# Kernel optimization log

Hardware: AMD Instinct MI355X
Metric: run time of the kernel (lower is better)

Reference implementation:

```python
import jax, jax.numpy as jnp
import numpy as np

N, D, H = 24, 256, 8
F = D // H  # 32


def setup_inputs() -> dict:
    key = jax.random.key(0)
    ks = jax.random.split(key, 9)
    T = 8192
    x = jax.random.normal(ks[0], (T, N * D), dtype=jnp.float32)
    s = 0.02
    # Joint-specific query weights: (H, N, D, F); shared K/V: (H, D, F)
    Wq = jax.random.normal(ks[1], (H, N, D, F), dtype=jnp.float32) * s
    bq = jax.random.normal(ks[2], (H, N, F), dtype=jnp.float32) * s
    Wk = jax.random.normal(ks[3], (H, D, F), dtype=jnp.float32) * s
    bk = jax.random.normal(ks[4], (H, F), dtype=jnp.float32) * s
    Wv = jax.random.normal(ks[5], (H, D, F), dtype=jnp.float32) * s
    bv = jax.random.normal(ks[6], (H, F), dtype=jnp.float32) * s
    gamma = jnp.ones((N * D,), dtype=jnp.float32)
    beta = jnp.zeros((N * D,), dtype=jnp.float32)
    return {"x": x, "Wq": Wq, "bq": bq, "Wk": Wk, "bk": bk,
            "Wv": Wv, "bv": bv, "gamma": gamma, "beta": beta}


def reference(x, Wq, bq, Wk, bk, Wv, bv, gamma, beta):
    T = x.shape[0]
    xr = x.reshape(T, N, D)                                   # (T, N, D)
    # Shared K/V per head, joint-specific Q per head
    k = jnp.einsum('tnd,hdf->thnf', xr, Wk) + bk[None, :, None, :]
    v = jnp.einsum('tnd,hdf->thnf', xr, Wv) + bv[None, :, None, :]
    q = jnp.einsum('tnd,hndf->thnf', xr, Wq) + bq[None, :, :, :]
    scores = jnp.einsum('thnf,thmf->thnm', q, k) / jnp.sqrt(jnp.float32(F))
    attn = jax.nn.softmax(scores, axis=-1)                    # (T, H, N, N)
    out = jnp.einsum('thnm,thmf->thnf', attn, v)              # (T, H, N, F)
    # Concat heads -> (T, N, H*F) = (T, N, D)
    out = jnp.transpose(out, (0, 2, 1, 3)).reshape(T, N * D)
    # Dropout is identity in eval mode; residual + LayerNorm over N*D
    y = x + out
    mu = jnp.mean(y, axis=-1, keepdims=True)
    var = jnp.mean((y - mu) ** 2, axis=-1, keepdims=True)
    y = (y - mu) * jax.lax.rsqrt(var + 1e-5)
    return y * gamma + beta
```

## Files before the change

### kernel.cpp

```cpp
#include <hip/hip_runtime.h>

#define NT 8192
#define NJ 24
#define DD 256
#define NH 8
#define FF 32
#define C3 768

typedef __attribute__((ext_vector_type(8))) _Float16 f16x8;
typedef __attribute__((ext_vector_type(2))) _Float16 half2v;
typedef __attribute__((ext_vector_type(4))) float f32x4;

__device__ __forceinline__ unsigned short f2h(float f) {
    union { _Float16 h; unsigned short u; } c;
    c.h = (_Float16)f;
    return c.u;
}

__device__ __forceinline__ float dot2(unsigned int a, unsigned int b, float c) {
#if __has_builtin(__builtin_amdgcn_fdot2)
    return __builtin_amdgcn_fdot2(__builtin_bit_cast(half2v, a),
                                  __builtin_bit_cast(half2v, b), c, false);
#else
    half2v ha = __builtin_bit_cast(half2v, a);
    half2v hb = __builtin_bit_cast(half2v, b);
    return c + (float)ha[0] * (float)hb[0] + (float)ha[1] * (float)hb[1];
#endif
}

__device__ __forceinline__ void gload16(const void* g, void* l) {
    __builtin_amdgcn_global_load_lds(
        (const __attribute__((address_space(1))) unsigned int*)g,
        (__attribute__((address_space(3))) unsigned int*)l, 16, 0, 0);
}

__global__ void pack_w(const float* __restrict__ Wq, const float* __restrict__ Wk,
                       const float* __restrict__ Wv, unsigned short* __restrict__ wbt) {
    size_t idx = (size_t)blockIdx.x * 256 + threadIdx.x;
    const size_t total = (size_t)NJ * C3 * DD;
    if (idx >= total) return;
    int d = idx & 255;
    int rest = (int)(idx >> 8);
    int c = rest % C3;
    int n = rest / C3;
    float v;
    if (c < 256) {
        int h = c >> 5, f = c & 31;
        v = Wq[((((size_t)h * NJ + n) * DD) + d) * FF + f];
    } else if (c < 512) {
        int cc = c - 256; int h = cc >> 5, f = cc & 31;
        v = Wk[(((size_t)h * DD) + d) * FF + f];
    } else {
        int cc = c - 512; int h = cc >> 5, f = cc & 31;
        v = Wv[(((size_t)h * DD) + d) * FF + f];
    }
    wbt[idx] = f2h(v);
}

__global__ void pack_b(const float* __restrict__ bq, const float* __restrict__ bk,
                       const float* __restrict__ bv, float* __restrict__ bias) {
    int idx = blockIdx.x * 256 + threadIdx.x;
    if (idx >= NJ * C3) return;
    int c = idx % C3;
    int n = idx / C3;
    float v;
    if (c < 256) {
        int h = c >> 5, f = c & 31;
        v = bq[((h * NJ + n) * FF) + f];
    } else if (c < 512) {
        int cc = c - 256; int h = cc >> 5, f = cc & 31;
        v = bk[h * FF + f];
    } else {
        int cc = c - 512; int h = cc >> 5, f = cc & 31;
        v = bv[h * FF + f];
    }
    bias[idx] = v;
}

__global__ void pack_x(const float* __restrict__ x, unsigned short* __restrict__ xb) {
    size_t idx = (size_t)blockIdx.x * 256 + threadIdx.x;
    const size_t total = (size_t)NT * NJ * DD / 4;
    if (idx >= total) return;
    float4 v = ((const float4*)x)[idx];
    ushort4 h;
    h.x = f2h(v.x); h.y = f2h(v.y); h.z = f2h(v.z); h.w = f2h(v.w);
    ((ushort4*)xb)[idx] = h;
}

#define BM 128
#define BN 128

__global__ __launch_bounds__(256, 3)
void gemm_qkv(const unsigned short* __restrict__ xb, const unsigned short* __restrict__ wbt,
              const float* __restrict__ bias, unsigned short* __restrict__ qkv,
              int t0, int mbs) {
    const int nwg = gridDim.x;
    const int cpx = nwg >> 3;
    const int bid = blockIdx.x;
    const int swz = (bid & 7) * cpx + (bid >> 3);
    const int nb = swz % 6;
    const int rest = swz / 6;
    const int mb = rest % mbs;
    const int nj = rest / mbs;

    const int tid = threadIdx.x;
    const int wave = tid >> 6, lane = tid & 63;

    __shared__ unsigned short As[BM * 64];
    __shared__ unsigned short Bs[BN * 64];

    f32x4 acc[4][4];
    #pragma unroll
    for (int i = 0; i < 4; ++i)
        #pragma unroll
        for (int j = 0; j < 4; ++j)
            #pragma unroll
            for (int r = 0; r < 4; ++r) acc[i][j][r] = 0.f;

    const int trow0 = t0 + mb * BM;
    const char* srcA = (const char*)(xb + (size_t)trow0 * (NJ * DD) + nj * DD);
    const char* srcB = (const char*)(wbt + ((size_t)nj * C3 + (size_t)nb * BN) * DD);

    const int rg = lane >> 3;
    const int sc = (lane & 7) ^ rg;

    const int wr = (wave >> 1) * 64;
    const int wc = (wave & 1) * 64;
    const int lr = lane & 15;
    const int g  = lane >> 4;

    for (int kb = 0; kb < 4; ++kb) {
        #pragma unroll
        for (int i = 0; i < 4; ++i) {
            int row0 = wave * 32 + i * 8;
            gload16(srcA + (size_t)(row0 + rg) * (NJ * DD * 2) + kb * 128 + sc * 16,
                    (char*)As + row0 * 128);
        }
        #pragma unroll
        for (int i = 0; i < 4; ++i) {
            int row0 = wave * 32 + i * 8;
            gload16(srcB + (size_t)(row0 + rg) * (DD * 2) + kb * 128 + sc * 16,
                    (char*)Bs + row0 * 128);
        }
        __syncthreads();

        #pragma unroll
        for (int kk = 0; kk < 2; ++kk) {
            f16x8 a[4], b[4];
            #pragma unroll
            for (int i = 0; i < 4; ++i) {
                int row = wr + i * 16 + lr;
                int c16 = (kk * 4 + g) ^ (row & 7);
                a[i] = *(const f16x8*)((const char*)As + row * 128 + c16 * 16);
            }
            #pragma unroll
            for (int j = 0; j < 4; ++j) {
                int row = wc + j * 16 + lr;
                int c16 = (kk * 4 + g) ^ (row & 7);
                b[j] = *(const f16x8*)((const char*)Bs + row * 128 + c16 * 16);
            }
            #pragma unroll
            for (int i = 0; i < 4; ++i)
                #pragma unroll
                for (int j = 0; j < 4; ++j)
                    acc[i][j] = __builtin_amdgcn_mfma_f32_16x16x32_f16(a[i], b[j], acc[i][j], 0, 0, 0);
        }
        __syncthreads();
    }

    const int ln = lane & 15;
    const int lq = (lane >> 4) * 4;
    float bv[4];
    #pragma unroll
    for (int j = 0; j < 4; ++j)
        bv[j] = bias[nj * C3 + nb * BN + wc + j * 16 + ln];
    #pragma unroll
    for (int i = 0; i < 4; ++i) {
        #pragma unroll
        for (int r = 0; r < 4; ++r) {
            int trow = mb * BM + wr + i * 16 + lq + r;
            size_t base = ((size_t)trow * NJ + nj) * C3 + (size_t)nb * BN;
            #pragma unroll
            for (int j = 0; j < 4; ++j) {
                float val = acc[i][j][r] + bv[j];
                qkv[base + wc + j * 16 + ln] = f2h(val);
            }
        }
    }
}

__global__ __launch_bounds__(256, 4)
void attn_ln(const unsigned short* __restrict__ qkv, const float* __restrict__ x,
             const float* __restrict__ gamma, const float* __restrict__ beta,
             float* __restrict__ out, int t0) {
    const int tloc = blockIdx.x;
    const int t = t0 + tloc;
    const int tid = threadIdx.x;
    const int wave = tid >> 6, lane = tid & 63;

    __shared__ __align__(16) unsigned short kv[NJ * 512];
    __shared__ float red[8];
    __shared__ float stats[2];
    float4* os4 = (float4*)kv;

    const uint4* tok = (const uint4*)(qkv + (size_t)tloc * (NJ * C3));

    #pragma unroll
    for (int j = 0; j < 6; ++j) {
        int idx = tid + j * 256;
        int m = idx >> 6, r = idx & 63;
        ((uint4*)kv)[(m << 6) + r] = tok[m * 96 + 32 + r];
    }

    const bool active = tid < NH * NJ;
    const int h = active ? (tid / NJ) : 0;
    const int n = active ? (tid - h * NJ) : 0;
    unsigned int qp[16];
    if (active) {
        const uint4* qsrc = tok + n * 96 + h * 4;
        #pragma unroll
        for (int jj = 0; jj < 4; ++jj) {
            uint4 w = qsrc[jj];
            qp[jj * 4 + 0] = w.x; qp[jj * 4 + 1] = w.y;
            qp[jj * 4 + 2] = w.z; qp[jj * 4 + 3] = w.w;
        }
    }
    __syncthreads();

    half2v o2[16];
    if (active) {
        const unsigned short* kbase = kv + h * FF;
        float s[NJ];
        float mx = -1e30f;
        #pragma unroll
        for (int m = 0; m < NJ; ++m) {
            const uint4* kp = (const uint4*)(kbase + m * 512);
            float a = 0.f;
            #pragma unroll
            for (int jj = 0; jj < 4; ++jj) {
                uint4 kw = kp[jj];
                a = dot2(kw.x, qp[jj * 4 + 0], a);
                a = dot2(kw.y, qp[jj * 4 + 1], a);
                a = dot2(kw.z, qp[jj * 4 + 2], a);
                a = dot2(kw.w, qp[jj * 4 + 3], a);
            }
            a *= 0.17677669529663687f;
            s[m] = a;
            mx = fmaxf(mx, a);
        }
        float sum = 0.f;
        #pragma unroll
        for (int m = 0; m < NJ; ++m) { s[m] = __expf(s[m] - mx); sum += s[m]; }
        float inv = 1.f / sum;
        #pragma unroll
        for (int k = 0; k < 16; ++k) o2[k] = half2v{(_Float16)0.f, (_Float16)0.f};
        const unsigned short* vbase = kv + 256 + h * FF;
        #pragma unroll
        for (int m = 0; m < NJ; ++m) {
            float wm = s[m] * inv;
            half2v wv = __builtin_bit_cast(half2v, __builtin_amdgcn_cvt_pkrtz(wm, wm));
            const uint4* vp = (const uint4*)(vbase + m * 512);
            #pragma unroll
            for (int jj = 0; jj < 4; ++jj) {
                uint4 vw = vp[jj];
                o2[jj * 4 + 0] += __builtin_bit_cast(half2v, vw.x) * wv;
                o2[jj * 4 + 1] += __builtin_bit_cast(half2v, vw.y) * wv;
                o2[jj * 4 + 2] += __builtin_bit_cast(half2v, vw.z) * wv;
                o2[jj * 4 + 3] += __builtin_bit_cast(half2v, vw.w) * wv;
            }
        }
    }
    __syncthreads();
    if (active) {
        int base4 = n * 64 + h * 8;
        #pragma unroll
        for (int jj = 0; jj < 8; ++jj) {
            int wi = base4 + jj;
            int sw = wi ^ ((wi >> 6) & 7);
            os4[sw] = make_float4((float)o2[jj * 2][0], (float)o2[jj * 2][1],
                                  (float)o2[jj * 2 + 1][0], (float)o2[jj * 2 + 1][1]);
        }
    }
    __syncthreads();

    const float4* x4 = (const float4*)(x + (size_t)t * (NJ * DD));
    float4 yv[6];
    float sum = 0.f, sq = 0.f;
    #pragma unroll
    for (int j = 0; j < 6; ++j) {
        int ri = tid + j * 256;
        float4 a = x4[ri];
        float4 b = os4[ri ^ ((ri >> 6) & 7)];
        float4 y;
        y.x = a.x + b.x; y.y = a.y + b.y; y.z = a.z + b.z; y.w = a.w + b.w;
        yv[j] = y;
        sum += y.x + y.y + y.z + y.w;
        sq  += y.x * y.x + y.y * y.y + y.z * y.z + y.w * y.w;
    }
    #pragma unroll
    for (int off = 32; off > 0; off >>= 1) {
        sum += __shfl_down(sum, off);
        sq  += __shfl_down(sq, off);
    }
    if (lane == 0) { red[wave] = sum; red[4 + wave] = sq; }
    __syncthreads();
    if (tid == 0) {
        float s = red[0] + red[1] + red[2] + red[3];
        float q = red[4] + red[5] + red[6] + red[7];
        float mu = s * (1.f / 6144.f);
        float var = q * (1.f / 6144.f) - mu * mu;
        stats[0] = mu;
        stats[1] = rsqrtf(var + 1e-5f);
    }
    __syncthreads();
    const float mu = stats[0], rs = stats[1];
    const float4* g4 = (const float4*)gamma;
    const float4* b4 = (const float4*)beta;
    float4* out4 = (float4*)(out + (size_t)t * (NJ * DD));
    #pragma unroll
    for (int j = 0; j < 6; ++j) {
        float4 g = g4[tid + j * 256];
        float4 bb = b4[tid + j * 256];
        float4 y = yv[j];
        y.x = (y.x - mu) * rs * g.x + bb.x;
        y.y = (y.y - mu) * rs * g.y + bb.y;
        y.z = (y.z - mu) * rs * g.z + bb.z;
        y.w = (y.w - mu) * rs * g.w + bb.w;
        out4[tid + j * 256] = y;
    }
}

extern "C" void kernel_launch(void* const* d_in, const int* in_sizes, int n_in,
                              void* d_out, int out_size, void* d_ws, size_t ws_size,
                              hipStream_t stream) {
    const float* x     = (const float*)d_in[0];
    const float* Wq    = (const float*)d_in[1];
    const float* bq    = (const float*)d_in[2];
    const float* Wk    = (const float*)d_in[3];
    const float* bk    = (const float*)d_in[4];
    const float* Wv    = (const float*)d_in[5];
    const float* bv    = (const float*)d_in[6];
    const float* gamma = (const float*)d_in[7];
    const float* beta  = (const float*)d_in[8];
    float* out = (float*)d_out;

    char* ws = (char*)d_ws;
    const size_t wbt_bytes  = (size_t)NJ * C3 * DD * 2;
    const size_t bias_bytes = (size_t)NJ * C3 * 4;
    const size_t xb_bytes   = (size_t)NT * NJ * DD * 2;
    unsigned short* wbt = (unsigned short*)ws;
    float* bias = (float*)(ws + wbt_bytes);
    unsigned short* xb  = (unsigned short*)(ws + wbt_bytes + bias_bytes);
    unsigned short* qkv = (unsigned short*)(ws + wbt_bytes + bias_bytes + xb_bytes);

    const size_t fixed = wbt_bytes + bias_bytes + xb_bytes;
    size_t avail = (ws_size > fixed) ? ws_size - fixed : 0;
    int chunk = NT;
    while (chunk > BM && (size_t)chunk * NJ * C3 * 2 > avail) chunk >>= 1;

    const size_t wtotal = (size_t)NJ * C3 * DD;
    pack_w<<<dim3((unsigned)((wtotal + 255) / 256)), dim3(256), 0, stream>>>(Wq, Wk, Wv, wbt);
    pack_b<<<dim3((NJ * C3 + 255) / 256), dim3(256), 0, stream>>>(bq, bk, bv, bias);
    const size_t xtotal4 = (size_t)NT * NJ * DD / 4;
    pack_x<<<dim3((unsigned)((xtotal4 + 255) / 256)), dim3(256), 0, stream>>>(x, xb);

    for (int t0 = 0; t0 < NT; t0 += chunk) {
        int mbs = chunk / BM;
        gemm_qkv<<<dim3(6 * mbs * NJ), dim3(256), 0, stream>>>(xb, wbt, bias, qkv, t0, mbs);
        attn_ln<<<dim3(chunk), dim3(256), 0, stream>>>(qkv, x, gamma, beta, out, t0);
    }
}
```

Baseline: 620.1 us.

## Fuse fp32-to-fp16 conversion of x into GEMM A-tile load and merge pack kernels

Removes the separate pack_x pass that wrote a half-precision copy of x. The QKV GEMM now loads fp32 x directly with float4 reads, converts to fp16 in registers and stores into swizzled LDS. Bias packing is folded into the weight pack kernel, saving a launch. This drops a full read and write of x through HBM. In exchange, each A tile is read at fp32 width six times (once per N-block) through synchronous register loads instead of async global_load_lds, which may stall the GEMM.

```diff
diff --git a/kernel.cpp b/kernel.cpp
--- a/kernel.cpp
+++ b/kernel.cpp
@@ -34,8 +34,10 @@
         (__attribute__((address_space(3))) unsigned int*)l, 16, 0, 0);
 }
 
-__global__ void pack_w(const float* __restrict__ Wq, const float* __restrict__ Wk,
-                       const float* __restrict__ Wv, unsigned short* __restrict__ wbt) {
+__global__ void pack_wb(const float* __restrict__ Wq, const float* __restrict__ Wk,
+                        const float* __restrict__ Wv, unsigned short* __restrict__ wbt,
+                        const float* __restrict__ bq, const float* __restrict__ bk,
+                        const float* __restrict__ bv, float* __restrict__ bias) {
     size_t idx = (size_t)blockIdx.x * 256 + threadIdx.x;
     const size_t total = (size_t)NJ * C3 * DD;
     if (idx >= total) return;
@@ -55,43 +57,30 @@
         v = Wv[(((size_t)h * DD) + d) * FF + f];
     }
     wbt[idx] = f2h(v);
-}
-
-__global__ void pack_b(const float* __restrict__ bq, const float* __restrict__ bk,
-                       const float* __restrict__ bv, float* __restrict__ bias) {
-    int idx = blockIdx.x * 256 + threadIdx.x;
-    if (idx >= NJ * C3) return;
-    int c = idx % C3;
-    int n = idx / C3;
-    float v;
-    if (c < 256) {
-        int h = c >> 5, f = c & 31;
-        v = bq[((h * NJ + n) * FF) + f];
-    } else if (c < 512) {
-        int cc = c - 256; int h = cc >> 5, f = cc & 31;
-        v = bk[h * FF + f];
-    } else {
-        int cc = c - 512; int h = cc >> 5, f = cc & 31;
-        v = bv[h * FF + f];
-    }
-    bias[idx] = v;
-}
-
-__global__ void pack_x(const float* __restrict__ x, unsigned short* __restrict__ xb) {
-    size_t idx = (size_t)blockIdx.x * 256 + threadIdx.x;
-    const size_t total = (size_t)NT * NJ * DD / 4;
-    if (idx >= total) return;
-    float4 v = ((const float4*)x)[idx];
-    ushort4 h;
-    h.x = f2h(v.x); h.y = f2h(v.y); h.z = f2h(v.z); h.w = f2h(v.w);
-    ((ushort4*)xb)[idx] = h;
+
+    if (idx < NJ * C3) {
+        int cb = (int)(idx % C3);
+        int nb2 = (int)(idx / C3);
+        float bvv;
+        if (cb < 256) {
+            int h = cb >> 5, f = cb & 31;
+            bvv = bq[((h * NJ + nb2) * FF) + f];
+        } else if (cb < 512) {
+            int cc = cb - 256; int h = cc >> 5, f = cc & 31;
+            bvv = bk[h * FF + f];
+        } else {
+            int cc = cb - 512; int h = cc >> 5, f = cc & 31;
+            bvv = bv[h * FF + f];
+        }
+        bias[idx] = bvv;
+    }
 }
 
 #define BM 128
 #define BN 128
 
 __global__ __launch_bounds__(256, 3)
-void gemm_qkv(const unsigned short* __restrict__ xb, const unsigned short* __restrict__ wbt,
+void gemm_qkv(const float* __restrict__ x, const unsigned short* __restrict__ wbt,
               const float* __restrict__ bias, unsigned short* __restrict__ qkv,
               int t0, int mbs) {
     const int nwg = gridDim.x;
@@ -118,7 +107,7 @@
             for (int r = 0; r < 4; ++r) acc[i][j][r] = 0.f;
 
     const int trow0 = t0 + mb * BM;
-    const char* srcA = (const char*)(xb + (size_t)trow0 * (NJ * DD) + nj * DD);
+    const float* srcA = x + (size_t)trow0 * (NJ * DD) + nj * DD;
     const char* srcB = (const char*)(wbt + ((size_t)nj * C3 + (size_t)nb * BN) * DD);
 
     const int rg = lane >> 3;
@@ -133,14 +122,27 @@
         #pragma unroll
         for (int i = 0; i < 4; ++i) {
             int row0 = wave * 32 + i * 8;
-            gload16(srcA + (size_t)(row0 + rg) * (NJ * DD * 2) + kb * 128 + sc * 16,
-                    (char*)As + row0 * 128);
-        }
-        #pragma unroll
-        for (int i = 0; i < 4; ++i) {
-            int row0 = wave * 32 + i * 8;
             gload16(srcB + (size_t)(row0 + rg) * (DD * 2) + kb * 128 + sc * 16,
                     (char*)Bs + row0 * 128);
+        }
+        {
+            const float* srcAk = srcA + kb * 64;
+            #pragma unroll
+            for (int it = 0; it < 4; ++it) {
+                int q = it * 256 + tid;
+                int row = q >> 3;
+                int c16 = q & 7;
+                const float* p = srcAk + (size_t)row * (NJ * DD) + c16 * 8;
+                float4 v0 = *(const float4*)p;
+                float4 v1 = *(const float4*)(p + 4);
+                f16x8 hv;
+                hv[0] = (_Float16)v0.x; hv[1] = (_Float16)v0.y;
+                hv[2] = (_Float16)v0.z; hv[3] = (_Float16)v0.w;
+                hv[4] = (_Float16)v1.x; hv[5] = (_Float16)v1.y;
+                hv[6] = (_Float16)v1.z; hv[7] = (_Float16)v1.w;
+                int c16s = c16 ^ (row & 7);
+                *(f16x8*)((char*)As + row * 128 + c16s * 16) = hv;
+            }
         }
         __syncthreads();
 
@@ -347,26 +349,22 @@
     char* ws = (char*)d_ws;
     const size_t wbt_bytes  = (size_t)NJ * C3 * DD * 2;
     const size_t bias_bytes = (size_t)NJ * C3 * 4;
-    const size_t xb_bytes   = (size_t)NT * NJ * DD * 2;
     unsigned short* wbt = (unsigned short*)ws;
     float* bias = (float*)(ws + wbt_bytes);
-    unsigned short* xb  = (unsigned short*)(ws + wbt_bytes + bias_bytes);
-    unsigned short* qkv = (unsigned short*)(ws + wbt_bytes + bias_bytes + xb_bytes);
-
-    const size_t fixed = wbt_bytes + bias_bytes + xb_bytes;
+    unsigned short* qkv = (unsigned short*)(ws + wbt_bytes + bias_bytes);
+
+    const size_t fixed = wbt_bytes + bias_bytes;
     size_t avail = (ws_size > fixed) ? ws_size - fixed : 0;
     int chunk = NT;
     while (chunk > BM && (size_t)chunk * NJ * C3 * 2 > avail) chunk >>= 1;
 
     const size_t wtotal = (size_t)NJ * C3 * DD;
-    pack_w<<<dim3((unsigned)((wtotal + 255) / 256)), dim3(256), 0, stream>>>(Wq, Wk, Wv, wbt);
-    pack_b<<<dim3((NJ * C3 + 255) / 256), dim3(256), 0, stream>>>(bq, bk, bv, bias);
-    const size_t xtotal4 = (size_t)NT * NJ * DD / 4;
-    pack_x<<<dim3((unsigned)((xtotal4 + 255) / 256)), dim3(256), 0, stream>>>(x, xb);
+    pack_wb<<<dim3((unsigned)((wtotal + 255) / 256)), dim3(256), 0, stream>>>(
+        Wq, Wk, Wv, wbt, bq, bk, bv, bias);
 
     for (int t0 = 0; t0 < NT; t0 += chunk) {
         int mbs = chunk / BM;
-        gemm_qkv<<<dim3(6 * mbs * NJ), dim3(256), 0, stream>>>(xb, wbt, bias, qkv, t0, mbs);
+        gemm_qkv<<<dim3(6 * mbs * NJ), dim3(256), 0, stream>>>(x, wbt, bias, qkv, t0, mbs);
         attn_ln<<<dim3(chunk), dim3(256), 0, stream>>>(qkv, x, gamma, beta, out, t0);
     }
 }
```

New measurement: 628.0 us. No clear change (+1.3%).
